# Kernel optimization log

Hardware: AMD Instinct MI355X
Metric: run time of the kernel (lower is better)

Reference implementation:

```python
import jax, jax.numpy as jnp
import numpy as np
from jax import lax

B, C, H, W = 8, 256, 128, 128
NH = 8
HD = C // NH
EPS = 1e-5


def setup_inputs() -> dict:
    key = jax.random.key(0)
    ks = jax.random.split(key, 6)
    x = jax.random.normal(ks[0], (B, C, H, W), dtype=jnp.float32)
    dw_weight = jax.random.normal(ks[1], (C, 1, 3, 3), dtype=jnp.float32) * 0.1
    off_weight = jax.random.normal(ks[2], (NH * 2, C), dtype=jnp.float32) * 0.05
    off_bias = jnp.zeros((NH * 2,), dtype=jnp.float32)
    v_weight = jax.random.normal(ks[3], (C, C), dtype=jnp.float32) * (1.0 / np.sqrt(C))
    o_weight = jax.random.normal(ks[4], (C, C), dtype=jnp.float32) * (1.0 / np.sqrt(C))
    gamma = jnp.ones((C,), dtype=jnp.float32)
    beta = jnp.zeros((C,), dtype=jnp.float32)
    return {"x": x, "dw_weight": dw_weight, "off_weight": off_weight, "off_bias": off_bias,
            "v_weight": v_weight, "o_weight": o_weight, "gamma": gamma, "beta": beta}


def reference(x, dw_weight, off_weight, off_bias, v_weight, o_weight, gamma, beta):
    b, c, h, w = x.shape
    # --- offset branch: depthwise 3x3 + pointwise 1x1 ---
    hdw = lax.conv_general_dilated(x, dw_weight, (1, 1), 'SAME',
                                   feature_group_count=c,
                                   dimension_numbers=('NCHW', 'OIHW', 'NCHW'))
    offsets = jnp.einsum('bchw,oc->bohw', hdw, off_weight) + off_bias[None, :, None, None]
    offsets = jnp.tanh(offsets) * 0.5                      # (B, 2*NH, H, W)
    offsets = offsets.reshape(b, NH, 2, h, w)
    dy, dx = offsets[:, :, 0], offsets[:, :, 1]            # (B, NH, H, W)

    # --- value projection, split into heads ---
    V = jnp.einsum('bchw,oc->bohw', x, v_weight).reshape(b, NH, HD, h, w)

    # --- deformable bilinear sampling (grid_sample, align_corners=True, border pad) ---
    gy = jnp.linspace(-1.0, 1.0, h, dtype=x.dtype)[None, None, :, None]
    gx = jnp.linspace(-1.0, 1.0, w, dtype=x.dtype)[None, None, None, :]
    sx = jnp.clip(gx + dx, -1.0, 1.0)                      # (B, NH, H, W)
    sy = jnp.clip(gy + dy, -1.0, 1.0)
    ix = (sx + 1.0) * 0.5 * (w - 1)                        # unnormalized coords
    iy = (sy + 1.0) * 0.5 * (h - 1)
    x0f = jnp.floor(ix); y0f = jnp.floor(iy)
    wx = ix - x0f; wy = iy - y0f
    x0 = jnp.clip(x0f.astype(jnp.int32), 0, w - 1)
    x1 = jnp.clip(x0f.astype(jnp.int32) + 1, 0, w - 1)
    y0 = jnp.clip(y0f.astype(jnp.int32), 0, h - 1)
    y1 = jnp.clip(y0f.astype(jnp.int32) + 1, 0, h - 1)

    Vf = V.reshape(b, NH, HD, h * w)

    def gather(yi, xi):
        idx = (yi * w + xi).reshape(b, NH, 1, h * w)
        return jnp.take_along_axis(Vf, idx, axis=3)        # (B, NH, HD, H*W)

    wx_ = wx.reshape(b, NH, 1, h * w); wy_ = wy.reshape(b, NH, 1, h * w)
    sampled = (gather(y0, x0) * (1 - wx_) * (1 - wy_)
               + gather(y0, x1) * wx_ * (1 - wy_)
               + gather(y1, x0) * (1 - wx_) * wy_
               + gather(y1, x1) * wx_ * wy_)
    out = sampled.reshape(b, c, h, w)

    # --- output projection + GroupNorm(NH groups) + residual ---
    out = jnp.einsum('bchw,oc->bohw', out, o_weight)
    g = out.reshape(b, NH, HD * h * w)
    mu = jnp.mean(g, axis=-1, keepdims=True)
    var = jnp.mean(jnp.square(g - mu), axis=-1, keepdims=True)
    g = (g - mu) * lax.rsqrt(var + EPS)
    out = g.reshape(b, c, h, w) * gamma[None, :, None, None] + beta[None, :, None, None]
    return x + out
```

## Files before the change

kernel.cpp:

```cpp
#include <hip/hip_runtime.h>
#include <hip/hip_bf16.h>

#define B_ 8
#define C_ 256
#define H_ 128
#define W_ 128
#define HW_ 16384
#define CHW_ (C_ * HW_)
#define NH_ 8
#define HD_ 32
#define NTOT (B_ * CHW_)

typedef short short8 __attribute__((ext_vector_type(8)));
typedef float f32x4 __attribute__((ext_vector_type(4)));

__global__ __launch_bounds__(256) void wconv_kernel(const float* __restrict__ vw,
                                                    const float* __restrict__ ow,
                                                    __hip_bfloat16* __restrict__ wvb,
                                                    __hip_bfloat16* __restrict__ wob) {
    int i = blockIdx.x * 256 + threadIdx.x;
    wvb[i] = __float2bfloat16(vw[i]);
    wob[i] = __float2bfloat16(ow[i]);
}

__global__ __launch_bounds__(256) void xt_kernel(const float* __restrict__ x,
                                                 __hip_bfloat16* __restrict__ xT) {
    __shared__ float tile[64][68];
    int t = threadIdx.x;
    int p0 = blockIdx.x * 64, c0 = blockIdx.y * 64, b = blockIdx.z;
    const float* xb = x + ((size_t)b * C_ + c0) * HW_ + p0;
#pragma unroll
    for (int l = 0; l < 4; ++l) {
        int idx = t + 256 * l;
        int row = idx >> 4, cf = idx & 15;
        float4 v = *(const float4*)&xb[(size_t)row * HW_ + cf * 4];
        *(float4*)&tile[row][cf * 4] = v;
    }
    __syncthreads();
    __hip_bfloat16* op = xT + ((size_t)b * HW_ + p0) * C_ + c0;
#pragma unroll
    for (int l = 0; l < 2; ++l) {
        int idx = t + 256 * l;
        int p = idx & 63, oct = idx >> 6;
        __hip_bfloat16 arr[8];
#pragma unroll
        for (int j = 0; j < 8; ++j) arr[j] = __float2bfloat16(tile[oct * 8 + j][p]);
        *(int4*)(op + (size_t)p * C_ + oct * 8) = *(int4*)arr;
    }
}

__global__ __launch_bounds__(256) void fused_offset_kernel(const float* __restrict__ x,
                                                           const float* __restrict__ dww,
                                                           const float* __restrict__ offw,
                                                           float* __restrict__ partials) {
    __shared__ float xt[4][10][136];
    __shared__ float wT[32][16];
    __shared__ float wd[32][9];
    int t = threadIdx.x;
    int rt = blockIdx.x, cg = blockIdx.y, b = blockIdx.z;
    int h0 = rt * 8, c0 = cg * 32;
    for (int i = t; i < 512; i += 256) { int o = i >> 5, c = i & 31; wT[c][o] = offw[o * 256 + c0 + c]; }
    for (int i = t; i < 288; i += 256) { wd[i / 9][i % 9] = dww[(c0 + i / 9) * 9 + i % 9]; }
    const float* xb = x + ((size_t)b * C_ + c0) * HW_;
    int col = t & 127;
    int sb = (t >> 7) * 4;
    float acc[4][16] = {};
    for (int cc0 = 0; cc0 < 32; cc0 += 4) {
        __syncthreads();
#pragma unroll
        for (int l = 0; l < 5; ++l) {
            int idx = t + 256 * l;
            int pr = idx >> 5, c4 = idx & 31;
            int cc = pr / 10, r = pr - cc * 10;
            int gh = h0 - 1 + r;
            float4 v = make_float4(0.f, 0.f, 0.f, 0.f);
            if (gh >= 0 && gh < H_)
                v = *(const float4*)&xb[(size_t)(cc0 + cc) * HW_ + gh * W_ + c4 * 4];
            *(float4*)&xt[cc][r][4 + c4 * 4] = v;
        }
        if (t < 80) { int pr = t >> 1, side = t & 1; xt[pr / 10][pr % 10][side ? 132 : 3] = 0.f; }
        __syncthreads();
#pragma unroll
        for (int cc = 0; cc < 4; ++cc) {
            float win[6][3];
#pragma unroll
            for (int rr = 0; rr < 6; ++rr)
#pragma unroll
                for (int kk = 0; kk < 3; ++kk)
                    win[rr][kk] = xt[cc][sb + rr][col + 3 + kk];
            float w9[9];
#pragma unroll
            for (int k9 = 0; k9 < 9; ++k9) w9[k9] = wd[cc0 + cc][k9];
#pragma unroll
            for (int j = 0; j < 4; ++j) {
                float s = 0.f;
#pragma unroll
                for (int ky = 0; ky < 3; ++ky)
#pragma unroll
                    for (int kx = 0; kx < 3; ++kx)
                        s += win[j + ky][kx] * w9[ky * 3 + kx];
#pragma unroll
                for (int o = 0; o < 16; ++o) acc[j][o] += s * wT[cc0 + cc][o];
            }
        }
    }
    float* pb = partials + (size_t)(cg * 8 + b) * 16 * HW_;
#pragma unroll
    for (int o = 0; o < 16; ++o)
#pragma unroll
        for (int j = 0; j < 4; ++j)
            pb[(size_t)o * HW_ + (h0 + sb + j) * W_ + col] = acc[j][o];
}

__global__ __launch_bounds__(256) void offreduce_kernel(const float* __restrict__ partials,
                                                        const float* __restrict__ offb,
                                                        float* __restrict__ off_buf) {
    int i = blockIdx.x * 256 + threadIdx.x;
    float s = 0.f;
#pragma unroll
    for (int cg = 0; cg < 8; ++cg) s += partials[(size_t)cg * 2097152 + i];
    int o = (i >> 14) & 15;
    off_buf[i] = tanhf(s + offb[o]) * 0.5f;
}

template<bool TRANS, bool STATS>
__global__ __launch_bounds__(256, 4) void mfma_gemm(const __hip_bfloat16* __restrict__ Wb,
                                                    const __hip_bfloat16* __restrict__ Xt,
                                                    void* __restrict__ Y,
                                                    float* __restrict__ stats) {
    __shared__ __align__(16) short smem[17408];
    int t = threadIdx.x;
    int wave = t >> 6, lane = t & 63;
    int quad = lane >> 4, l16 = lane & 15;
    int b = blockIdx.z;
    int n0 = blockIdx.x * 128, m0 = blockIdx.y * 128;
    const short* Wp = (const short*)Wb + (size_t)m0 * 256;
    const short* Xp = (const short*)Xt + ((size_t)b * HW_ + n0) * 256;

    int i0 = t, i1 = t + 256;
    int r0 = i0 >> 2, r1 = i1 >> 2;
    int ss0 = (i0 & 3) ^ ((r0 >> 1) & 3);
    int ss1 = (i1 & 3) ^ ((r1 >> 1) & 3);

#define STAGE(buf, ko)                                                                                          \
    do {                                                                                                        \
        short* Asm_ = smem + (buf) * 4096;                                                                      \
        short* Bsm_ = smem + 8192 + (buf) * 4096;                                                               \
        __builtin_amdgcn_global_load_lds(Wp + (size_t)r0 * 256 + (ko) + ss0 * 8, Asm_ + i0 * 8, 16, 0, 0);      \
        __builtin_amdgcn_global_load_lds(Wp + (size_t)r1 * 256 + (ko) + ss1 * 8, Asm_ + i1 * 8, 16, 0, 0);      \
        __builtin_amdgcn_global_load_lds(Xp + (size_t)r0 * 256 + (ko) + ss0 * 8, Bsm_ + i0 * 8, 16, 0, 0);      \
        __builtin_amdgcn_global_load_lds(Xp + (size_t)r1 * 256 + (ko) + ss1 * 8, Bsm_ + i1 * 8, 16, 0, 0);      \
    } while (0)

    f32x4 acc[2][8];
#pragma unroll
    for (int mt = 0; mt < 2; ++mt)
#pragma unroll
        for (int nt = 0; nt < 8; ++nt) acc[mt][nt] = (f32x4){0.f, 0.f, 0.f, 0.f};

    STAGE(0, 0);
    __syncthreads();

#pragma unroll
    for (int kk = 0; kk < 8; ++kk) {
        int cur = kk & 1;
        if (kk < 7) STAGE(cur ^ 1, (kk + 1) * 32);
        __builtin_amdgcn_sched_barrier(0);
        const short* Ac = smem + cur * 4096;
        const short* Bc = smem + 8192 + cur * 4096;
        short8 af[2], bf[8];
#pragma unroll
        for (int mt = 0; mt < 2; ++mt) {
            int r = wave * 32 + mt * 16 + l16;
            int sl = quad ^ ((r >> 1) & 3);
            af[mt] = *(const short8*)&Ac[r * 32 + sl * 8];
        }
#pragma unroll
        for (int nt = 0; nt < 8; ++nt) {
            int r = nt * 16 + l16;
            int sl = quad ^ ((r >> 1) & 3);
            bf[nt] = *(const short8*)&Bc[r * 32 + sl * 8];
        }
#pragma unroll
        for (int mt = 0; mt < 2; ++mt)
#pragma unroll
            for (int nt = 0; nt < 8; ++nt)
                acc[mt][nt] = __builtin_amdgcn_mfma_f32_16x16x32_bf16(af[mt], bf[nt], acc[mt][nt], 0, 0, 0);
        __syncthreads();
    }
#undef STAGE

    if constexpr (TRANS) {
#pragma unroll
        for (int mt = 0; mt < 2; ++mt)
#pragma unroll
            for (int nt = 0; nt < 8; ++nt) {
                int n = nt * 16 + l16;
                int mloc = wave * 32 + mt * 16 + quad * 4;
                __hip_bfloat16 arr[4];
#pragma unroll
                for (int r = 0; r < 4; ++r) arr[r] = __float2bfloat16(acc[mt][nt][r]);
                *(int2*)&smem[n * 136 + mloc] = *(int2*)arr;
            }
        __syncthreads();
        short* Yb = (short*)Y + (size_t)b * CHW_;
#pragma unroll
        for (int i = 0; i < 8; ++i) {
            int id = t + 256 * i;
            int row = id >> 4, c = id & 15;
            int4 v = *(const int4*)&smem[row * 136 + c * 8];
            *(int4*)(Yb + (size_t)(n0 + row) * 256 + m0 + c * 8) = v;
        }
    } else {
        float* Yb = (float*)Y + (size_t)b * CHW_;
#pragma unroll
        for (int mt = 0; mt < 2; ++mt)
#pragma unroll
            for (int nt = 0; nt < 8; ++nt)
#pragma unroll
                for (int r = 0; r < 4; ++r) {
                    int m = m0 + wave * 32 + mt * 16 + quad * 4 + r;
                    int n = n0 + nt * 16 + l16;
                    Yb[(size_t)m * HW_ + n] = acc[mt][nt][r];
                }
    }
    if constexpr (STATS) {
        float s1 = 0.f, s2 = 0.f;
#pragma unroll
        for (int mt = 0; mt < 2; ++mt)
#pragma unroll
            for (int nt = 0; nt < 8; ++nt)
#pragma unroll
                for (int r = 0; r < 4; ++r) {
                    float v = acc[mt][nt][r];
                    s1 += v;
                    s2 += v * v;
                }
#pragma unroll
        for (int o = 32; o; o >>= 1) {
            s1 += __shfl_down(s1, o);
            s2 += __shfl_down(s2, o);
        }
        if (lane == 0) {
            int grp = b * NH_ + (m0 >> 5) + wave;
            atomicAdd(&stats[grp * 2 + 0], s1);
            atomicAdd(&stats[grp * 2 + 1], s2);
        }
    }
}

__global__ __launch_bounds__(256) void sample_kernel(const __hip_bfloat16* __restrict__ VT,
                                                     const float* __restrict__ off,
                                                     __hip_bfloat16* __restrict__ sT) {
    int t = threadIdx.x;
    int chunk = t & 3;
    int g = t >> 2;
    int head = g & 7;
    int p = blockIdx.x * 8 + (g >> 3);
    int b = blockIdx.z;
    int h = p >> 7, w = p & 127;
    const float* ob = off + ((size_t)b * 16 + head * 2) * HW_ + p;
    float dy = ob[0], dx = ob[HW_];
    float gy = h * (2.0f / 127.0f) - 1.0f;
    float gx = w * (2.0f / 127.0f) - 1.0f;
    float sx = fminf(fmaxf(gx + dx, -1.0f), 1.0f);
    float sy = fminf(fmaxf(gy + dy, -1.0f), 1.0f);
    float ix = (sx + 1.0f) * 0.5f * 127.0f;
    float iy = (sy + 1.0f) * 0.5f * 127.0f;
    float x0f = floorf(ix), y0f = floorf(iy);
    float wx = ix - x0f, wy = iy - y0f;
    int x0 = min(max((int)x0f, 0), 127);
    int x1 = min((int)x0f + 1, 127);
    int y0 = min(max((int)y0f, 0), 127);
    int y1 = min((int)y0f + 1, 127);
    float w00 = (1.f - wx) * (1.f - wy), w01 = wx * (1.f - wy);
    float w10 = (1.f - wx) * wy, w11 = wx * wy;
    const short* Vb = (const short*)VT + (size_t)b * CHW_ + head * 32 + chunk * 8;
    short8 v00 = *(const short8*)(Vb + (size_t)(y0 * W_ + x0) * C_);
    short8 v01 = *(const short8*)(Vb + (size_t)(y0 * W_ + x1) * C_);
    short8 v10 = *(const short8*)(Vb + (size_t)(y1 * W_ + x0) * C_);
    short8 v11 = *(const short8*)(Vb + (size_t)(y1 * W_ + x1) * C_);
    __hip_bfloat16 arr[8];
#pragma unroll
    for (int j = 0; j < 8; ++j) {
        float f = __bfloat162float(((const __hip_bfloat16*)&v00)[j]) * w00 +
                  __bfloat162float(((const __hip_bfloat16*)&v01)[j]) * w01 +
                  __bfloat162float(((const __hip_bfloat16*)&v10)[j]) * w10 +
                  __bfloat162float(((const __hip_bfloat16*)&v11)[j]) * w11;
        arr[j] = __float2bfloat16(f);
    }
    __hip_bfloat16* op = sT + ((size_t)b * HW_ + p) * C_ + head * 32 + chunk * 8;
    *(int4*)op = *(int4*)arr;
}

__global__ __launch_bounds__(256) void final_kernel(const float* __restrict__ x,
                                                    const float* __restrict__ stats,
                                                    const float* __restrict__ gamma,
                                                    const float* __restrict__ beta,
                                                    float* __restrict__ out) {
    int idx = (blockIdx.x * 256 + threadIdx.x) * 4;
    int c = (idx >> 14) & 255;
    int b = idx >> 22;
    int grp = b * NH_ + (c >> 5);
    const float invN = 1.0f / (float)(HD_ * HW_);
    float mu = stats[grp * 2 + 0] * invN;
    float var = stats[grp * 2 + 1] * invN - mu * mu;
    float r = rsqrtf(var + 1e-5f);
    float g = gamma[c], be = beta[c];
    float4 v = *(const float4*)&out[idx];
    float4 xv = *(const float4*)&x[idx];
    float4 o;
    o.x = xv.x + (v.x - mu) * r * g + be;
    o.y = xv.y + (v.y - mu) * r * g + be;
    o.z = xv.z + (v.z - mu) * r * g + be;
    o.w = xv.w + (v.w - mu) * r * g + be;
    *(float4*)&out[idx] = o;
}

extern "C" void kernel_launch(void* const* d_in, const int* in_sizes, int n_in,
                              void* d_out, int out_size, void* d_ws, size_t ws_size,
                              hipStream_t stream) {
    const float* x     = (const float*)d_in[0];
    const float* dww   = (const float*)d_in[1];
    const float* offw  = (const float*)d_in[2];
    const float* offb  = (const float*)d_in[3];
    const float* vw    = (const float*)d_in[4];
    const float* ow    = (const float*)d_in[5];
    const float* gamma = (const float*)d_in[6];
    const float* beta  = (const float*)d_in[7];
    float* out = (float*)d_out;
    float* ws_f = (float*)d_ws;

    float* partials = ws_f;
    float* off_buf  = ws_f + 16777216;
    float* stats    = ws_f + 18874368;
    __hip_bfloat16* wvb = (__hip_bfloat16*)(ws_f + 18874624);
    __hip_bfloat16* wob = wvb + 65536;
    __hip_bfloat16* xT  = (__hip_bfloat16*)(ws_f + 18940160);
    __hip_bfloat16* sT  = (__hip_bfloat16*)partials;
    __hip_bfloat16* vT  = (__hip_bfloat16*)out;

    wconv_kernel<<<256, 256, 0, stream>>>(vw, ow, wvb, wob);
    xt_kernel<<<dim3(256, 4, 8), 256, 0, stream>>>(x, xT);
    fused_offset_kernel<<<dim3(16, 8, 8), 256, 0, stream>>>(x, dww, offw, partials);
    offreduce_kernel<<<8192, 256, 0, stream>>>(partials, offb, off_buf);
    mfma_gemm<true, false><<<dim3(128, 2, 8), 256, 0, stream>>>(wvb, xT, (void*)vT, nullptr);
    sample_kernel<<<dim3(2048, 1, 8), 256, 0, stream>>>(vT, off_buf, sT);
    hipMemsetAsync(stats, 0, 128 * sizeof(float), stream);
    mfma_gemm<false, true><<<dim3(128, 2, 8), 256, 0, stream>>>(wob, sT, (void*)out, stats);
    final_kernel<<<NTOT / 1024, 256, 0, stream>>>(x, stats, gamma, beta, out);
}
```

Baseline: 558.3 us.

## Widen GEMM tile to full 256 output channels and use fast tanh

Both 1x1-conv GEMMs now use 512-thread blocks that each cover all 256 output channels for a 128-pixel tile. Each activation tile is loaded once instead of twice, and the launch grid halves. The transposed epilogue is split into two 64-row halves so it fits the enlarged shared buffer. The offset tanh is replaced by an exp2-based fast formula, which trades a little accuracy for fewer instructions; the larger blocks also raise register and LDS pressure per CU.

```diff
diff --git a/kernel.cpp b/kernel.cpp
--- a/kernel.cpp
+++ b/kernel.cpp
@@ -120,36 +120,39 @@
 #pragma unroll
     for (int cg = 0; cg < 8; ++cg) s += partials[(size_t)cg * 2097152 + i];
     int o = (i >> 14) & 15;
-    off_buf[i] = tanhf(s + offb[o]) * 0.5f;
+    float z = s + offb[o];
+    float e = exp2f(z * 2.885390082f);
+    off_buf[i] = (1.0f - __fdividef(2.0f, e + 1.0f)) * 0.5f;
 }
 
 template<bool TRANS, bool STATS>
-__global__ __launch_bounds__(256, 4) void mfma_gemm(const __hip_bfloat16* __restrict__ Wb,
+__global__ __launch_bounds__(512, 6) void mfma_gemm(const __hip_bfloat16* __restrict__ Wb,
                                                     const __hip_bfloat16* __restrict__ Xt,
                                                     void* __restrict__ Y,
                                                     float* __restrict__ stats) {
-    __shared__ __align__(16) short smem[17408];
+    __shared__ __align__(16) short smem[24576];
     int t = threadIdx.x;
     int wave = t >> 6, lane = t & 63;
     int quad = lane >> 4, l16 = lane & 15;
     int b = blockIdx.z;
-    int n0 = blockIdx.x * 128, m0 = blockIdx.y * 128;
-    const short* Wp = (const short*)Wb + (size_t)m0 * 256;
+    int n0 = blockIdx.x * 128;
+    const short* Wp = (const short*)Wb;
     const short* Xp = (const short*)Xt + ((size_t)b * HW_ + n0) * 256;
 
-    int i0 = t, i1 = t + 256;
-    int r0 = i0 >> 2, r1 = i1 >> 2;
-    int ss0 = (i0 & 3) ^ ((r0 >> 1) & 3);
-    int ss1 = (i1 & 3) ^ ((r1 >> 1) & 3);
+    int iA0 = t, iA1 = t + 512;
+    int rA0 = iA0 >> 2, rA1 = iA1 >> 2;
+    int sA0 = (iA0 & 3) ^ ((rA0 >> 1) & 3);
+    int sA1 = (iA1 & 3) ^ ((rA1 >> 1) & 3);
+    int rB0 = t >> 2;
+    int sB0 = (t & 3) ^ ((rB0 >> 1) & 3);
 
 #define STAGE(buf, ko)                                                                                          \
     do {                                                                                                        \
-        short* Asm_ = smem + (buf) * 4096;                                                                      \
-        short* Bsm_ = smem + 8192 + (buf) * 4096;                                                               \
-        __builtin_amdgcn_global_load_lds(Wp + (size_t)r0 * 256 + (ko) + ss0 * 8, Asm_ + i0 * 8, 16, 0, 0);      \
-        __builtin_amdgcn_global_load_lds(Wp + (size_t)r1 * 256 + (ko) + ss1 * 8, Asm_ + i1 * 8, 16, 0, 0);      \
-        __builtin_amdgcn_global_load_lds(Xp + (size_t)r0 * 256 + (ko) + ss0 * 8, Bsm_ + i0 * 8, 16, 0, 0);      \
-        __builtin_amdgcn_global_load_lds(Xp + (size_t)r1 * 256 + (ko) + ss1 * 8, Bsm_ + i1 * 8, 16, 0, 0);      \
+        short* Asm_ = smem + (buf) * 8192;                                                                      \
+        short* Bsm_ = smem + 16384 + (buf) * 4096;                                                              \
+        __builtin_amdgcn_global_load_lds(Wp + (size_t)rA0 * 256 + (ko) + sA0 * 8, Asm_ + iA0 * 8, 16, 0, 0);    \
+        __builtin_amdgcn_global_load_lds(Wp + (size_t)rA1 * 256 + (ko) + sA1 * 8, Asm_ + iA1 * 8, 16, 0, 0);    \
+        __builtin_amdgcn_global_load_lds(Xp + (size_t)rB0 * 256 + (ko) + sB0 * 8, Bsm_ + t * 8, 16, 0, 0);      \
     } while (0)
 
     f32x4 acc[2][8];
@@ -166,8 +169,8 @@
         int cur = kk & 1;
         if (kk < 7) STAGE(cur ^ 1, (kk + 1) * 32);
         __builtin_amdgcn_sched_barrier(0);
-        const short* Ac = smem + cur * 4096;
-        const short* Bc = smem + 8192 + cur * 4096;
+        const short* Ac = smem + cur * 8192;
+        const short* Bc = smem + 16384 + cur * 4096;
         short8 af[2], bf[8];
 #pragma unroll
         for (int mt = 0; mt < 2; ++mt) {
@@ -191,25 +194,30 @@
 #undef STAGE
 
     if constexpr (TRANS) {
-#pragma unroll
-        for (int mt = 0; mt < 2; ++mt)
-#pragma unroll
-            for (int nt = 0; nt < 8; ++nt) {
-                int n = nt * 16 + l16;
-                int mloc = wave * 32 + mt * 16 + quad * 4;
-                __hip_bfloat16 arr[4];
-#pragma unroll
-                for (int r = 0; r < 4; ++r) arr[r] = __float2bfloat16(acc[mt][nt][r]);
-                *(int2*)&smem[n * 136 + mloc] = *(int2*)arr;
+        short* Yb = (short*)Y + (size_t)b * CHW_;
+#pragma unroll
+        for (int h = 0; h < 2; ++h) {
+#pragma unroll
+            for (int mt = 0; mt < 2; ++mt)
+#pragma unroll
+                for (int q = 0; q < 4; ++q) {
+                    int nt = h * 4 + q;
+                    int nr = q * 16 + l16;
+                    int mloc = wave * 32 + mt * 16 + quad * 4;
+                    __hip_bfloat16 arr[4];
+#pragma unroll
+                    for (int r = 0; r < 4; ++r) arr[r] = __float2bfloat16(acc[mt][nt][r]);
+                    *(int2*)&smem[nr * 264 + mloc] = *(int2*)arr;
+                }
+            __syncthreads();
+#pragma unroll
+            for (int j = 0; j < 4; ++j) {
+                int id = t + 512 * j;
+                int row = id >> 5, c = id & 31;
+                int4 v = *(const int4*)&smem[row * 264 + c * 8];
+                *(int4*)(Yb + (size_t)(n0 + h * 64 + row) * 256 + c * 8) = v;
             }
-        __syncthreads();
-        short* Yb = (short*)Y + (size_t)b * CHW_;
-#pragma unroll
-        for (int i = 0; i < 8; ++i) {
-            int id = t + 256 * i;
-            int row = id >> 4, c = id & 15;
-            int4 v = *(const int4*)&smem[row * 136 + c * 8];
-            *(int4*)(Yb + (size_t)(n0 + row) * 256 + m0 + c * 8) = v;
+            __syncthreads();
         }
     } else {
         float* Yb = (float*)Y + (size_t)b * CHW_;
@@ -219,7 +227,7 @@
             for (int nt = 0; nt < 8; ++nt)
 #pragma unroll
                 for (int r = 0; r < 4; ++r) {
-                    int m = m0 + wave * 32 + mt * 16 + quad * 4 + r;
+                    int m = wave * 32 + mt * 16 + quad * 4 + r;
                     int n = n0 + nt * 16 + l16;
                     Yb[(size_t)m * HW_ + n] = acc[mt][nt][r];
                 }
@@ -242,7 +250,7 @@
             s2 += __shfl_down(s2, o);
         }
         if (lane == 0) {
-            int grp = b * NH_ + (m0 >> 5) + wave;
+            int grp = b * NH_ + wave;
             atomicAdd(&stats[grp * 2 + 0], s1);
             atomicAdd(&stats[grp * 2 + 1], s2);
         }
@@ -344,9 +352,9 @@
     xt_kernel<<<dim3(256, 4, 8), 256, 0, stream>>>(x, xT);
     fused_offset_kernel<<<dim3(16, 8, 8), 256, 0, stream>>>(x, dww, offw, partials);
     offreduce_kernel<<<8192, 256, 0, stream>>>(partials, offb, off_buf);
-    mfma_gemm<true, false><<<dim3(128, 2, 8), 256, 0, stream>>>(wvb, xT, (void*)vT, nullptr);
+    mfma_gemm<true, false><<<dim3(128, 1, 8), 512, 0, stream>>>(wvb, xT, (void*)vT, nullptr);
     sample_kernel<<<dim3(2048, 1, 8), 256, 0, stream>>>(vT, off_buf, sT);
     hipMemsetAsync(stats, 0, 128 * sizeof(float), stream);
-    mfma_gemm<false, true><<<dim3(128, 2, 8), 256, 0, stream>>>(wob, sT, (void*)out, stats);
+    mfma_gemm<false, true><<<dim3(128, 1, 8), 512, 0, stream>>>(wob, sT, (void*)out, stats);
     final_kernel<<<NTOT / 1024, 256, 0, stream>>>(x, stats, gamma, beta, out);
 }
```

Result: slower. 885.5 us (+58.6%).
